# Optimization experiments

Hardware: AMD Instinct MI355X
Metric: run time of the kernel (lower is better)

The kernel has to match this reference:

```python
import jax, jax.numpy as jnp
import numpy as np
import math

B, S, D, H, DFF = 4, 2048, 1024, 16, 4096
DK = D // H
EPS = 1e-5

def setup_inputs() -> dict:
    key = jax.random.key(0)
    ks = jax.random.split(key, 16)
    s_d = 1.0 / math.sqrt(D)
    s_ff = 1.0 / math.sqrt(DFF)
    return {
        "x": jax.random.normal(ks[0], (B, S, D), jnp.float32),
        "wq": jax.random.uniform(ks[1], (D, D), jnp.float32, -s_d, s_d),
        "bq": jnp.zeros((D,), jnp.float32),
        "wk": jax.random.uniform(ks[2], (D, D), jnp.float32, -s_d, s_d),
        "bk": jnp.zeros((D,), jnp.float32),
        "wv": jax.random.uniform(ks[3], (D, D), jnp.float32, -s_d, s_d),
        "bv": jnp.zeros((D,), jnp.float32),
        "wo": jax.random.uniform(ks[4], (D, D), jnp.float32, -s_d, s_d),
        "bo": jnp.zeros((D,), jnp.float32),
        "w1": jax.random.uniform(ks[5], (DFF, D), jnp.float32, -s_d, s_d),
        "b1": jnp.zeros((DFF,), jnp.float32),
        "w2": jax.random.uniform(ks[6], (D, DFF), jnp.float32, -s_ff, s_ff),
        "b2": jnp.zeros((D,), jnp.float32),
        "ln1_g": jnp.ones((D,), jnp.float32),
        "ln1_b": jnp.zeros((D,), jnp.float32),
        "ln2_g": jnp.ones((D,), jnp.float32),
        "ln2_b": jnp.zeros((D,), jnp.float32),
    }

def _layernorm(x, g, b):
    mu = jnp.mean(x, axis=-1, keepdims=True)
    var = jnp.mean(jnp.square(x - mu), axis=-1, keepdims=True)
    return (x - mu) * jax.lax.rsqrt(var + EPS) * g + b

def reference(x, wq, bq, wk, bk, wv, bv, wo, bo, w1, b1, w2, b2, ln1_g, ln1_b, ln2_g, ln2_b):
    # Multi-head self-attention (dropout in eval mode -> identity).
    Q = (x @ wq.T + bq).reshape(B, S, H, DK).transpose(0, 2, 1, 3)  # (B,H,S,DK)
    K = (x @ wk.T + bk).reshape(B, S, H, DK).transpose(0, 2, 1, 3)
    V = (x @ wv.T + bv).reshape(B, S, H, DK).transpose(0, 2, 1, 3)
    scores = jnp.einsum('bhqd,bhkd->bhqk', Q, K) / math.sqrt(DK)  # (B,H,S,S)
    attn = jax.nn.softmax(scores, axis=-1)
    ctx = jnp.einsum('bhqk,bhkd->bhqd', attn, V)
    ctx = ctx.transpose(0, 2, 1, 3).reshape(B, S, D)
    attn_out = ctx @ wo.T + bo
    # SkipConnection: x + norm(sublayer)  (post-applied LayerNorm on sublayer output)
    x = x + _layernorm(attn_out, ln1_g, ln1_b)
    # FFN
    ff = jax.nn.relu(x @ w1.T + b1) @ w2.T + b2
    return x + _layernorm(ff, ln2_g, ln2_b)
```

## Files before the change

kernel.cpp:

```cpp
#include <hip/hip_runtime.h>
#include <hip/hip_bf16.h>
#include <stdint.h>


#define DI __device__ __forceinline__

typedef __attribute__((ext_vector_type(4))) float f32x4;
typedef __attribute__((ext_vector_type(16))) float f32x16;
typedef __attribute__((ext_vector_type(8))) short bf16x8;
typedef __attribute__((ext_vector_type(4))) short s16x4;

#define B_ 4
#define S_ 2048
#define D_ 1024
#define H_ 16
#define DK_ 64
#define DFF_ 4096
#define M_ 8192

DI float bf2f(short s) {
  union { unsigned u; float f; } v;
  v.u = ((unsigned)(unsigned short)s) << 16;
  return v.f;
}
DI short f2bf(float f) {
  union { float f; unsigned u; } v;
  v.f = f;
  unsigned r = v.u + 0x7FFFu + ((v.u >> 16) & 1u);
  return (short)(r >> 16);
}
DI unsigned pkbf(float lo, float hi) {
  unsigned r;
  asm("v_cvt_pk_bf16_f32 %0, %1, %2" : "=v"(r) : "v"(lo), "v"(hi));
  return r;
}
DI void plswap(unsigned& a, unsigned& b) {
  asm volatile("v_permlane32_swap_b32 %0, %1" : "+v"(a), "+v"(b));
}
DI float ex2(float x) {
  float r;
  asm("v_exp_f32 %0, %1" : "=v"(r) : "v"(x));
  return r;
}

__global__ __launch_bounds__(256) void cvt_kernel(const float* __restrict__ in,
                                                  short* __restrict__ out, int n) {
  long i = ((long)blockIdx.x * blockDim.x + threadIdx.x) * 8;
  if (i >= n) return;
  f32x4 a = *(const f32x4*)(in + i);
  f32x4 b = *(const f32x4*)(in + i + 4);
  bf16x8 r;
  r[0] = f2bf(a[0]); r[1] = f2bf(a[1]); r[2] = f2bf(a[2]); r[3] = f2bf(a[3]);
  r[4] = f2bf(b[0]); r[5] = f2bf(b[1]); r[6] = f2bf(b[2]); r[7] = f2bf(b[3]);
  *(bf16x8*)(out + i) = r;
}

DI void gl_lds16(const void* g, void* l) {
  __builtin_amdgcn_global_load_lds(
      (const __attribute__((address_space(1))) unsigned int*)g,
      (__attribute__((address_space(3))) unsigned int*)l, 16, 0, 0);
}

template <int BN, int MODE>
__global__ __launch_bounds__(512, 2)
void gemm_qs(const short* __restrict__ A, const short* __restrict__ Bm,
             const float* __restrict__ bias0, const float* __restrict__ bias1,
             const float* __restrict__ bias2, short* __restrict__ C,
             int M, int N, int K,
             short* __restrict__ Qo, short* __restrict__ Ko, short* __restrict__ Vo) {
  constexpr int NF = BN / 64;
  constexpr int WN = BN / 4;
  constexpr int ASLOT = 256 * 32;
  constexpr int BSLOT = BN * 32;

  __shared__ short As[4 * ASLOT];
  __shared__ short Bs[4 * BSLOT];

  const int t = threadIdx.x, w = t >> 6, l = t & 63;
  const int wm = w >> 2, wn = w & 3;
  const int lr = l & 15, lk = l >> 4;

  const int gx = gridDim.x;
  const int nwg = gx * gridDim.y;
  const int orig = blockIdx.y * gx + blockIdx.x;
  const int lin = (orig & 7) * (nwg >> 3) + (orig >> 3);
  const int row0 = (lin / gx) * 256;
  const int col0 = (lin % gx) * BN;

  const int NT = K >> 5;

  const int r0 = t >> 2, s0 = (((t & 3) ^ ((r0 >> 1) & 3)) << 3);
  const int r1 = r0 + 128, s1 = (((t & 3) ^ ((r1 >> 1) & 3)) << 3);
  const short* Asrc0 = A + (long)(row0 + r0) * K + s0;
  const short* Asrc1 = A + (long)(row0 + r1) * K + s1;
  const short* Bsrc0 = Bm + (long)(col0 + r0) * K + s0;
  const short* Bsrc1 = Bm + (long)(col0 + r1) * K + s1;
  const int d0 = t * 8, d1 = (t + 512) * 8;

  auto stageA = [&](int kt) {
    const int ko = kt << 5;
    short* Ab = As + (kt & 3) * ASLOT;
    gl_lds16(Asrc0 + ko, Ab + d0);
    gl_lds16(Asrc1 + ko, Ab + d1);
  };
  auto stageB = [&](int kt) {
    const int ko = kt << 5;
    short* Bb = Bs + (kt & 3) * BSLOT;
    gl_lds16(Bsrc0 + ko, Bb + d0);
    if constexpr (BN == 256) gl_lds16(Bsrc1 + ko, Bb + d1);
  };

  f32x4 acc[8][NF] = {};

  stageA(0); stageB(0);
  stageA(1); stageB(1);
  stageA(2); stageB(2);

  for (int kt = 0; kt < NT; ++kt) {
    if (kt + 2 < NT) {
      if constexpr (BN == 256) asm volatile("s_waitcnt vmcnt(8)" ::: "memory");
      else                     asm volatile("s_waitcnt vmcnt(6)" ::: "memory");
    } else if (kt + 1 < NT) {
      if constexpr (BN == 256) asm volatile("s_waitcnt vmcnt(4)" ::: "memory");
      else                     asm volatile("s_waitcnt vmcnt(3)" ::: "memory");
    } else {
      asm volatile("s_waitcnt vmcnt(0)" ::: "memory");
    }
    __builtin_amdgcn_s_barrier();

    const short* aw = As + (kt & 3) * ASLOT + wm * (128 * 32);
    const short* bw = Bs + (kt & 3) * BSLOT + wn * (WN * 32);

    bf16x8 afr[4], bfr[NF];
#pragma unroll
    for (int m = 0; m < 4; ++m) {
      const int rr = m * 16 + lr;
      afr[m] = *(const bf16x8*)(aw + rr * 32 + ((lk ^ ((rr >> 1) & 3)) << 3));
    }
#pragma unroll
    for (int n = 0; n < NF; ++n) {
      const int rr = n * 16 + lr;
      bfr[n] = *(const bf16x8*)(bw + rr * 32 + ((lk ^ ((rr >> 1) & 3)) << 3));
    }
    if (kt + 3 < NT) stageA(kt + 3);
    __builtin_amdgcn_s_barrier();
    asm volatile("s_waitcnt lgkmcnt(0)" ::: "memory");
    __builtin_amdgcn_sched_barrier(0);
    __builtin_amdgcn_s_setprio(1);
#pragma unroll
    for (int m = 0; m < 4; ++m)
#pragma unroll
      for (int n = 0; n < NF; ++n)
        acc[m][n] =
            __builtin_amdgcn_mfma_f32_16x16x32_bf16(afr[m], bfr[n], acc[m][n], 0, 0, 0);
    __builtin_amdgcn_s_setprio(0);

    bf16x8 af2[4];
#pragma unroll
    for (int m = 0; m < 4; ++m) {
      const int rr = 64 + m * 16 + lr;
      af2[m] = *(const bf16x8*)(aw + rr * 32 + ((lk ^ ((rr >> 1) & 3)) << 3));
    }
    if (kt + 3 < NT) stageB(kt + 3);
    __builtin_amdgcn_s_barrier();
    asm volatile("s_waitcnt lgkmcnt(0)" ::: "memory");
    __builtin_amdgcn_sched_barrier(0);
    __builtin_amdgcn_s_setprio(1);
#pragma unroll
    for (int m = 0; m < 4; ++m)
#pragma unroll
      for (int n = 0; n < NF; ++n)
        acc[4 + m][n] =
            __builtin_amdgcn_mfma_f32_16x16x32_bf16(af2[m], bfr[n], acc[4 + m][n], 0, 0, 0);
    __builtin_amdgcn_s_setprio(0);
  }

  if (MODE == 2) {
    const int which = col0 >> 10;
#pragma unroll
    for (int m = 0; m < 8; ++m) {
#pragma unroll
      for (int n = 0; n < NF; ++n) {
        const int r0e = row0 + wm * 128 + m * 16 + lk * 4;
        const int c = col0 + wn * WN + n * 16 + lr;
        const int cc = c & 1023;
        const int h = cc >> 6, dk = cc & 63;
        const int bb = r0e >> 11, s = r0e & 2047;
        if (which == 2) {
          const float bias = bias2[cc];
          s16x4 v4;
#pragma unroll
          for (int j = 0; j < 4; ++j) v4[j] = f2bf(acc[m][n][j] + bias);
          *(s16x4*)(Vo + ((long)((bb * H_ + h) * DK_ + dk)) * S_ + s) = v4;
        } else {
          const float bias = (which == 0 ? bias0[cc] : bias1[cc]);
          const float sc = (which == 0 ? 0.1803368801f : 1.0f);
          short* dst = (which == 0 ? Qo : Ko);
#pragma unroll
          for (int j = 0; j < 4; ++j)
            dst[(((long)(bb * H_ + h) * S_) + s + j) * DK_ + dk] =
                f2bf((acc[m][n][j] + bias) * sc);
        }
      }
    }
  } else {
#pragma unroll
    for (int m = 0; m < 8; ++m) {
#pragma unroll
      for (int n = 0; n < NF; ++n) {
#pragma unroll
        for (int j = 0; j < 4; ++j) {
          const int r = row0 + wm * 128 + m * 16 + lk * 4 + j;
          const int c = col0 + wn * WN + n * 16 + lr;
          float v = acc[m][n][j] + bias0[c];
          if (MODE == 1) v = fmaxf(v, 0.0f);
          C[(long)r * N + c] = f2bf(v);
        }
      }
    }
  }
}

__global__ __launch_bounds__(256, 4)
void attn_kernel(const short* __restrict__ Q, const short* __restrict__ K,
                 const short* __restrict__ Vt, short* __restrict__ ctx) {
  __shared__ short Ks[2 * 64 * 64];
  __shared__ short Vs[2 * 64 * 64];
  const int t = threadIdx.x, w = t >> 6, l = t & 63;
  const int q31 = l & 31, hi = l >> 5;
  const int bh = blockIdx.y;
  const int q0 = blockIdx.x * 128 + w * 32;
  const long base = (long)bh * S_ * DK_;

  bf16x8 qf[4];
  {
    const short* qp = Q + base + (long)(q0 + q31) * DK_ + hi * 8;
#pragma unroll
    for (int ks = 0; ks < 4; ++ks) qf[ks] = *(const bf16x8*)(qp + ks * 16);
  }

  f32x16 oa[2] = {};
  float mrun = -1e30f, lrun = 0.0f;

  const int srow = l >> 3;
  const int scol = ((l & 7) ^ srow) * 8;
  const int kr0 = w * 16 + srow, kr1 = w * 16 + 8 + srow;
  const int lw0 = w * 1024, lw1 = w * 1024 + 512;

  gl_lds16(K + base + (long)kr0 * DK_ + scol, &Ks[lw0]);
  gl_lds16(K + base + (long)kr1 * DK_ + scol, &Ks[lw1]);
  gl_lds16(Vt + base + (long)kr0 * S_ + scol, &Vs[lw0]);
  gl_lds16(Vt + base + (long)kr1 * S_ + scol, &Vs[lw1]);

  for (int tt = 0; tt < 32; ++tt) {
    asm volatile("s_waitcnt vmcnt(0)" ::: "memory");
    __builtin_amdgcn_s_barrier();
    if (tt + 1 < 32) {
      const int kb = ((tt + 1) & 1) * 4096;
      const int kvn = (tt + 1) * 64;
      gl_lds16(K + base + (long)(kvn + kr0) * DK_ + scol, &Ks[kb + lw0]);
      gl_lds16(K + base + (long)(kvn + kr1) * DK_ + scol, &Ks[kb + lw1]);
      gl_lds16(Vt + base + (long)kr0 * S_ + kvn + scol, &Vs[kb + lw0]);
      gl_lds16(Vt + base + (long)kr1 * S_ + kvn + scol, &Vs[kb + lw1]);
    }
    const int cb = (tt & 1) * 4096;

    f32x16 sacc[2] = {};
#pragma unroll
    for (int m = 0; m < 2; ++m) {
      const int row = m * 32 + q31;
      const int sw = row & 7;
#pragma unroll
      for (int ks = 0; ks < 4; ++ks) {
        bf16x8 kf = *(const bf16x8*)&Ks[cb + row * 64 + (((2 * ks + hi) ^ sw) << 3)];
        sacc[m] = __builtin_amdgcn_mfma_f32_32x32x16_bf16(kf, qf[ks], sacc[m], 0, 0, 0);
      }
    }

    float mx[8];
#pragma unroll
    for (int r = 0; r < 8; ++r)
      mx[r] = fmaxf(fmaxf(sacc[0][r], sacc[0][r + 8]),
                    fmaxf(sacc[1][r], sacc[1][r + 8]));
    mx[0] = fmaxf(mx[0], mx[4]); mx[1] = fmaxf(mx[1], mx[5]);
    mx[2] = fmaxf(mx[2], mx[6]); mx[3] = fmaxf(mx[3], mx[7]);
    float tm = fmaxf(fmaxf(mx[0], mx[1]), fmaxf(mx[2], mx[3]));
    tm = fmaxf(tm, __shfl_xor(tm, 32, 64));

    if (!__all(tm <= mrun + 8.0f)) {
      const float mnew = fmaxf(mrun, tm);
      const float fac = ex2(mrun - mnew);
      lrun *= fac;
#pragma unroll
      for (int m = 0; m < 2; ++m)
#pragma unroll
        for (int r = 0; r < 16; ++r) oa[m][r] *= fac;
      mrun = mnew;
    }

#pragma unroll
    for (int m = 0; m < 2; ++m)
#pragma unroll
      for (int r = 0; r < 16; ++r) sacc[m][r] = ex2(sacc[m][r] - mrun);

    float sm[8];
#pragma unroll
    for (int r = 0; r < 8; ++r)
      sm[r] = (sacc[0][r] + sacc[0][r + 8]) + (sacc[1][r] + sacc[1][r + 8]);
    sm[0] += sm[4]; sm[1] += sm[5]; sm[2] += sm[6]; sm[3] += sm[7];
    float ps = (sm[0] + sm[1]) + (sm[2] + sm[3]);
    ps += __shfl_xor(ps, 32, 64);
    lrun += ps;

    bf16x8 pf[4];
#pragma unroll
    for (int m = 0; m < 2; ++m)
#pragma unroll
      for (int sb = 0; sb < 2; ++sb) {
        unsigned p0 = pkbf(sacc[m][8 * sb + 0], sacc[m][8 * sb + 1]);
        unsigned p1 = pkbf(sacc[m][8 * sb + 2], sacc[m][8 * sb + 3]);
        unsigned p2 = pkbf(sacc[m][8 * sb + 4], sacc[m][8 * sb + 5]);
        unsigned p3 = pkbf(sacc[m][8 * sb + 6], sacc[m][8 * sb + 7]);
        plswap(p0, p2);
        plswap(p1, p3);
        union { unsigned u[4]; bf16x8 v; } fb;
        fb.u[0] = p0; fb.u[1] = p1; fb.u[2] = p2; fb.u[3] = p3;
        pf[2 * m + sb] = fb.v;
      }

#pragma unroll
    for (int mt = 0; mt < 2; ++mt) {
      const int row = mt * 32 + q31;
      const int sw = row & 7;
#pragma unroll
      for (int s = 0; s < 4; ++s) {
        bf16x8 vf = *(const bf16x8*)&Vs[cb + row * 64 + (((2 * s + hi) ^ sw) << 3)];
        oa[mt] = __builtin_amdgcn_mfma_f32_32x32x16_bf16(vf, pf[s], oa[mt], 0, 0, 0);
      }
    }
  }

  const int bb2 = bh >> 4, h = bh & 15;
  const float rl = 1.0f / lrun;
  short* crow = ctx + ((long)(bb2 * S_ + q0 + q31)) * D_ + h * 64 + 4 * hi;
#pragma unroll
  for (int mt = 0; mt < 2; ++mt)
#pragma unroll
    for (int g = 0; g < 4; ++g) {
      s16x4 v4;
#pragma unroll
      for (int i = 0; i < 4; ++i) v4[i] = f2bf(oa[mt][4 * g + i] * rl);
      *(s16x4*)(crow + mt * 32 + g * 8) = v4;
    }
}

template <int RES_BF16, int OUT_BF16>
__global__ __launch_bounds__(256)
void add_ln(const void* __restrict__ resv, const short* __restrict__ a,
            const float* __restrict__ gam, const float* __restrict__ bet,
            void* __restrict__ outv) {
  const int row = blockIdx.x, t = threadIdx.x;
  const int w = t >> 6, l = t & 63;
  const long roff = (long)row * D_;
  const int c = t * 4;
  s16x4 av = *(const s16x4*)(a + roff + c);
  float v0 = bf2f(av[0]), v1 = bf2f(av[1]), v2 = bf2f(av[2]), v3 = bf2f(av[3]);
  float s = v0 + v1 + v2 + v3;
#pragma unroll
  for (int mask = 1; mask < 64; mask <<= 1) s += __shfl_xor(s, mask, 64);
  __shared__ float r1[4], r2[4];
  if (l == 0) r1[w] = s;
  __syncthreads();
  float mu = (r1[0] + r1[1] + r1[2] + r1[3]) * (1.0f / D_);
  float d0 = v0 - mu, d1 = v1 - mu, d2 = v2 - mu, d3 = v3 - mu;
  float sq = d0 * d0 + d1 * d1 + d2 * d2 + d3 * d3;
#pragma unroll
  for (int mask = 1; mask < 64; mask <<= 1) sq += __shfl_xor(sq, mask, 64);
  if (l == 0) r2[w] = sq;
  __syncthreads();
  float var = (r2[0] + r2[1] + r2[2] + r2[3]) * (1.0f / D_);
  float rs = rsqrtf(var + 1e-5f);
  float res0, res1, res2, res3;
  if (RES_BF16) {
    s16x4 rv = *(const s16x4*)((const short*)resv + roff + c);
    res0 = bf2f(rv[0]); res1 = bf2f(rv[1]); res2 = bf2f(rv[2]); res3 = bf2f(rv[3]);
  } else {
    f32x4 rv = *(const f32x4*)((const float*)resv + roff + c);
    res0 = rv[0]; res1 = rv[1]; res2 = rv[2]; res3 = rv[3];
  }
  float o0 = res0 + d0 * rs * gam[c + 0] + bet[c + 0];
  float o1 = res1 + d1 * rs * gam[c + 1] + bet[c + 1];
  float o2 = res2 + d2 * rs * gam[c + 2] + bet[c + 2];
  float o3 = res3 + d3 * rs * gam[c + 3] + bet[c + 3];
  if (OUT_BF16) {
    s16x4 ov;
    ov[0] = f2bf(o0); ov[1] = f2bf(o1); ov[2] = f2bf(o2); ov[3] = f2bf(o3);
    *(s16x4*)((short*)outv + roff + c) = ov;
  } else {
    f32x4 ov;
    ov[0] = o0; ov[1] = o1; ov[2] = o2; ov[3] = o3;
    *(f32x4*)((float*)outv + roff + c) = ov;
  }
}

extern "C" void kernel_launch(void* const* d_in, const int* in_sizes, int n_in,
                              void* d_out, int out_size, void* d_ws, size_t ws_size,
                              hipStream_t stream) {
  (void)in_sizes; (void)n_in; (void)out_size; (void)ws_size;
  const float* x   = (const float*)d_in[0];
  const float* wq  = (const float*)d_in[1];
  const float* bq  = (const float*)d_in[2];
  const float* wk  = (const float*)d_in[3];
  const float* bk  = (const float*)d_in[4];
  const float* wv  = (const float*)d_in[5];
  const float* bv  = (const float*)d_in[6];
  const float* wo  = (const float*)d_in[7];
  const float* bo  = (const float*)d_in[8];
  const float* w1  = (const float*)d_in[9];
  const float* b1  = (const float*)d_in[10];
  const float* w2  = (const float*)d_in[11];
  const float* b2  = (const float*)d_in[12];
  const float* g1  = (const float*)d_in[13];
  const float* be1 = (const float*)d_in[14];
  const float* g2  = (const float*)d_in[15];
  const float* be2 = (const float*)d_in[16];

  char* ws = (char*)d_ws;
  const long MB = 1 << 20;
  short* xb    = (short*)(ws + 0 * MB);
  short* wqkvb = (short*)(ws + 16 * MB);
  short* wob   = (short*)(ws + 22 * MB);
  short* w1b   = (short*)(ws + 24 * MB);
  short* w2b   = (short*)(ws + 32 * MB);
  short* Qb    = (short*)(ws + 40 * MB);
  short* Kb    = (short*)(ws + 56 * MB);
  short* Vtb   = (short*)(ws + 72 * MB);
  short* ctxb  = (short*)(ws + 88 * MB);
  short* aout  = (short*)(ws + 40 * MB);
  short* x1b   = (short*)(ws + 56 * MB);
  short* hid   = (short*)(ws + 88 * MB);
  short* ffb   = (short*)(ws + 72 * MB);

  auto cvt = [&](const float* in, short* out, long n) {
    cvt_kernel<<<dim3((unsigned)((n / 8 + 255) / 256)), dim3(256), 0, stream>>>(in, out, (int)n);
  };
  cvt(x, xb, (long)M_ * D_);
  cvt(wq, wqkvb + 0L * D_ * D_, (long)D_ * D_);
  cvt(wk, wqkvb + 1L * D_ * D_, (long)D_ * D_);
  cvt(wv, wqkvb + 2L * D_ * D_, (long)D_ * D_);
  cvt(wo, wob, (long)D_ * D_);
  cvt(w1, w1b, (long)DFF_ * D_);
  cvt(w2, w2b, (long)D_ * DFF_);

  gemm_qs<256, 2><<<dim3(3072 / 256, M_ / 256), 512, 0, stream>>>(
      xb, wqkvb, bq, bk, bv, nullptr, M_, 3072, D_, Qb, Kb, Vtb);

  attn_kernel<<<dim3(S_ / 128, B_ * H_), 256, 0, stream>>>(Qb, Kb, Vtb, ctxb);

  gemm_qs<128, 0><<<dim3(D_ / 128, M_ / 256), 512, 0, stream>>>(
      ctxb, wob, bo, nullptr, nullptr, aout, M_, D_, D_, nullptr, nullptr, nullptr);

  add_ln<0, 1><<<dim3(M_), 256, 0, stream>>>(x, aout, g1, be1, x1b);

  gemm_qs<256, 1><<<dim3(DFF_ / 256, M_ / 256), 512, 0, stream>>>(
      x1b, w1b, b1, nullptr, nullptr, hid, M_, DFF_, D_, nullptr, nullptr, nullptr);
  gemm_qs<128, 0><<<dim3(D_ / 128, M_ / 256), 512, 0, stream>>>(
      hid, w2b, b2, nullptr, nullptr, ffb, M_, D_, DFF_, nullptr, nullptr, nullptr);

  add_ln<1, 0><<<dim3(M_), 256, 0, stream>>>(x1b, ffb, g2, be2, d_out);
}
```

Before: 419.5 us.

## Retile GEMM warp grid, enlarge attention blocks with XCD-aware mapping, use max3

For the BN=128 GEMMs the 8 waves are rearranged into a 4x2 grid, so each wave covers 64x64 instead of 128x32, which changes the balance of A and B fragment reads from LDS. The attention kernel moves to 512-thread blocks covering 256 queries, so each K/V tile staged in LDS is shared by twice as many waves. Its block index is remapped so that blocks of the same batch-head land on the same XCD, improving L2 reuse of K and V. The running-max reduction now uses v_max3_f32. The larger blocks raise per-block register and LDS pressure and may reduce the number of resident blocks.

Result: no change. 413.0 us (-1.5%).

```diff
diff --git a/kernel.cpp b/kernel.cpp
--- a/kernel.cpp
+++ b/kernel.cpp
@@ -40,6 +40,11 @@
 DI float ex2(float x) {
   float r;
   asm("v_exp_f32 %0, %1" : "=v"(r) : "v"(x));
+  return r;
+}
+DI float max3(float a, float b, float c) {
+  float r;
+  asm("v_max3_f32 %0, %1, %2, %3" : "=v"(r) : "v"(a), "v"(b), "v"(c));
   return r;
 }
 
@@ -61,6 +66,11 @@
       (__attribute__((address_space(3))) unsigned int*)l, 16, 0, 0);
 }
 
+#define VMCNT(N) asm volatile("s_waitcnt vmcnt(" #N ")" ::: "memory")
+#define LGKM0                                          \
+  asm volatile("s_waitcnt lgkmcnt(0)" ::: "memory");   \
+  __builtin_amdgcn_sched_barrier(0)
+
 template <int BN, int MODE>
 __global__ __launch_bounds__(512, 2)
 void gemm_qs(const short* __restrict__ A, const short* __restrict__ Bm,
@@ -68,8 +78,13 @@
              const float* __restrict__ bias2, short* __restrict__ C,
              int M, int N, int K,
              short* __restrict__ Qo, short* __restrict__ Ko, short* __restrict__ Vo) {
-  constexpr int NF = BN / 64;
-  constexpr int WN = BN / 4;
+  constexpr int WR = (BN == 256 ? 2 : 4);
+  constexpr int WC = 8 / WR;
+  constexpr int WM = 256 / WR;
+  constexpr int WN = BN / WC;
+  constexpr int MF = WM / 16;
+  constexpr int NFr = WN / 16;
+  constexpr int MH = MF / 2;
   constexpr int ASLOT = 256 * 32;
   constexpr int BSLOT = BN * 32;
 
@@ -77,7 +92,8 @@
   __shared__ short Bs[4 * BSLOT];
 
   const int t = threadIdx.x, w = t >> 6, l = t & 63;
-  const int wm = w >> 2, wn = w & 3;
+  const int wm = (WR == 2 ? (w >> 2) : (w >> 1));
+  const int wn = (WR == 2 ? (w & 3) : (w & 1));
   const int lr = l & 15, lk = l >> 4;
 
   const int gx = gridDim.x;
@@ -110,7 +126,7 @@
     if constexpr (BN == 256) gl_lds16(Bsrc1 + ko, Bb + d1);
   };
 
-  f32x4 acc[8][NF] = {};
+  f32x4 acc[MF][NFr] = {};
 
   stageA(0); stageB(0);
   stageA(1); stageB(1);
@@ -118,70 +134,66 @@
 
   for (int kt = 0; kt < NT; ++kt) {
     if (kt + 2 < NT) {
-      if constexpr (BN == 256) asm volatile("s_waitcnt vmcnt(8)" ::: "memory");
-      else                     asm volatile("s_waitcnt vmcnt(6)" ::: "memory");
+      if constexpr (BN == 256) VMCNT(8); else VMCNT(6);
     } else if (kt + 1 < NT) {
-      if constexpr (BN == 256) asm volatile("s_waitcnt vmcnt(4)" ::: "memory");
-      else                     asm volatile("s_waitcnt vmcnt(3)" ::: "memory");
+      if constexpr (BN == 256) VMCNT(4); else VMCNT(3);
     } else {
-      asm volatile("s_waitcnt vmcnt(0)" ::: "memory");
+      VMCNT(0);
     }
     __builtin_amdgcn_s_barrier();
 
-    const short* aw = As + (kt & 3) * ASLOT + wm * (128 * 32);
+    const short* aw = As + (kt & 3) * ASLOT + wm * (WM * 32);
     const short* bw = Bs + (kt & 3) * BSLOT + wn * (WN * 32);
 
-    bf16x8 afr[4], bfr[NF];
-#pragma unroll
-    for (int m = 0; m < 4; ++m) {
+    bf16x8 afr[MH], bfr[NFr];
+#pragma unroll
+    for (int m = 0; m < MH; ++m) {
       const int rr = m * 16 + lr;
       afr[m] = *(const bf16x8*)(aw + rr * 32 + ((lk ^ ((rr >> 1) & 3)) << 3));
     }
 #pragma unroll
-    for (int n = 0; n < NF; ++n) {
+    for (int n = 0; n < NFr; ++n) {
       const int rr = n * 16 + lr;
       bfr[n] = *(const bf16x8*)(bw + rr * 32 + ((lk ^ ((rr >> 1) & 3)) << 3));
     }
     if (kt + 3 < NT) stageA(kt + 3);
     __builtin_amdgcn_s_barrier();
-    asm volatile("s_waitcnt lgkmcnt(0)" ::: "memory");
-    __builtin_amdgcn_sched_barrier(0);
+    LGKM0;
     __builtin_amdgcn_s_setprio(1);
 #pragma unroll
-    for (int m = 0; m < 4; ++m)
-#pragma unroll
-      for (int n = 0; n < NF; ++n)
+    for (int m = 0; m < MH; ++m)
+#pragma unroll
+      for (int n = 0; n < NFr; ++n)
         acc[m][n] =
             __builtin_amdgcn_mfma_f32_16x16x32_bf16(afr[m], bfr[n], acc[m][n], 0, 0, 0);
     __builtin_amdgcn_s_setprio(0);
 
-    bf16x8 af2[4];
-#pragma unroll
-    for (int m = 0; m < 4; ++m) {
-      const int rr = 64 + m * 16 + lr;
+    bf16x8 af2[MH];
+#pragma unroll
+    for (int m = 0; m < MH; ++m) {
+      const int rr = (MH + m) * 16 + lr;
       af2[m] = *(const bf16x8*)(aw + rr * 32 + ((lk ^ ((rr >> 1) & 3)) << 3));
     }
     if (kt + 3 < NT) stageB(kt + 3);
     __builtin_amdgcn_s_barrier();
-    asm volatile("s_waitcnt lgkmcnt(0)" ::: "memory");
-    __builtin_amdgcn_sched_barrier(0);
+    LGKM0;
     __builtin_amdgcn_s_setprio(1);
 #pragma unroll
-    for (int m = 0; m < 4; ++m)
-#pragma unroll
-      for (int n = 0; n < NF; ++n)
-        acc[4 + m][n] =
-            __builtin_amdgcn_mfma_f32_16x16x32_bf16(af2[m], bfr[n], acc[4 + m][n], 0, 0, 0);
+    for (int m = 0; m < MH; ++m)
+#pragma unroll
+      for (int n = 0; n < NFr; ++n)
+        acc[MH + m][n] =
+            __builtin_amdgcn_mfma_f32_16x16x32_bf16(af2[m], bfr[n], acc[MH + m][n], 0, 0, 0);
     __builtin_amdgcn_s_setprio(0);
   }
 
   if (MODE == 2) {
     const int which = col0 >> 10;
 #pragma unroll
-    for (int m = 0; m < 8; ++m) {
-#pragma unroll
-      for (int n = 0; n < NF; ++n) {
-        const int r0e = row0 + wm * 128 + m * 16 + lk * 4;
+    for (int m = 0; m < MF; ++m) {
+#pragma unroll
+      for (int n = 0; n < NFr; ++n) {
+        const int r0e = row0 + wm * WM + m * 16 + lk * 4;
         const int c = col0 + wn * WN + n * 16 + lr;
         const int cc = c & 1023;
         const int h = cc >> 6, dk = cc & 63;
@@ -205,12 +217,12 @@
     }
   } else {
 #pragma unroll
-    for (int m = 0; m < 8; ++m) {
-#pragma unroll
-      for (int n = 0; n < NF; ++n) {
+    for (int m = 0; m < MF; ++m) {
+#pragma unroll
+      for (int n = 0; n < NFr; ++n) {
 #pragma unroll
         for (int j = 0; j < 4; ++j) {
-          const int r = row0 + wm * 128 + m * 16 + lk * 4 + j;
+          const int r = row0 + wm * WM + m * 16 + lk * 4 + j;
           const int c = col0 + wn * WN + n * 16 + lr;
           float v = acc[m][n][j] + bias0[c];
           if (MODE == 1) v = fmaxf(v, 0.0f);
@@ -221,15 +233,18 @@
   }
 }
 
-__global__ __launch_bounds__(256, 4)
+__global__ __launch_bounds__(512, 4)
 void attn_kernel(const short* __restrict__ Q, const short* __restrict__ K,
                  const short* __restrict__ Vt, short* __restrict__ ctx) {
-  __shared__ short Ks[2 * 64 * 64];
-  __shared__ short Vs[2 * 64 * 64];
+  __shared__ short Ks[2 * 4096];
+  __shared__ short Vs[2 * 4096];
   const int t = threadIdx.x, w = t >> 6, l = t & 63;
   const int q31 = l & 31, hi = l >> 5;
-  const int bh = blockIdx.y;
-  const int q0 = blockIdx.x * 128 + w * 32;
+
+  const int orig = blockIdx.y * gridDim.x + blockIdx.x;
+  const int xcd = orig & 7, k7 = orig >> 3;
+  const int bh = xcd * 8 + (k7 >> 3);
+  const int q0 = (k7 & 7) * 256 + w * 32;
   const long base = (long)bh * S_ * DK_;
 
   bf16x8 qf[4];
@@ -242,27 +257,24 @@
   f32x16 oa[2] = {};
   float mrun = -1e30f, lrun = 0.0f;
 
-  const int srow = l >> 3;
-  const int scol = ((l & 7) ^ srow) * 8;
-  const int kr0 = w * 16 + srow, kr1 = w * 16 + 8 + srow;
-  const int lw0 = w * 1024, lw1 = w * 1024 + 512;
-
-  gl_lds16(K + base + (long)kr0 * DK_ + scol, &Ks[lw0]);
-  gl_lds16(K + base + (long)kr1 * DK_ + scol, &Ks[lw1]);
-  gl_lds16(Vt + base + (long)kr0 * S_ + scol, &Vs[lw0]);
-  gl_lds16(Vt + base + (long)kr1 * S_ + scol, &Vs[lw1]);
+  const int trow = t >> 3;
+  const int tcol = (((t & 7) ^ (trow & 7)) << 3);
+  const short* Ksrc = K + base + (long)trow * DK_ + tcol;
+  const short* Vsrc = Vt + base + (long)trow * S_ + tcol;
+
+  auto stg = [&](int tile, int slot) {
+    const int kb = slot * 4096;
+    const int kvn = tile * 64;
+    gl_lds16(Ksrc + (long)kvn * DK_, &Ks[kb + t * 8]);
+    gl_lds16(Vsrc + kvn, &Vs[kb + t * 8]);
+  };
+
+  stg(0, 0);
 
   for (int tt = 0; tt < 32; ++tt) {
-    asm volatile("s_waitcnt vmcnt(0)" ::: "memory");
+    VMCNT(0);
     __builtin_amdgcn_s_barrier();
-    if (tt + 1 < 32) {
-      const int kb = ((tt + 1) & 1) * 4096;
-      const int kvn = (tt + 1) * 64;
-      gl_lds16(K + base + (long)(kvn + kr0) * DK_ + scol, &Ks[kb + lw0]);
-      gl_lds16(K + base + (long)(kvn + kr1) * DK_ + scol, &Ks[kb + lw1]);
-      gl_lds16(Vt + base + (long)kr0 * S_ + kvn + scol, &Vs[kb + lw0]);
-      gl_lds16(Vt + base + (long)kr1 * S_ + kvn + scol, &Vs[kb + lw1]);
-    }
+    if (tt + 1 < 32) stg(tt + 1, (tt + 1) & 1);
     const int cb = (tt & 1) * 4096;
 
     f32x16 sacc[2] = {};
@@ -280,11 +292,10 @@
     float mx[8];
 #pragma unroll
     for (int r = 0; r < 8; ++r)
-      mx[r] = fmaxf(fmaxf(sacc[0][r], sacc[0][r + 8]),
-                    fmaxf(sacc[1][r], sacc[1][r + 8]));
-    mx[0] = fmaxf(mx[0], mx[4]); mx[1] = fmaxf(mx[1], mx[5]);
-    mx[2] = fmaxf(mx[2], mx[6]); mx[3] = fmaxf(mx[3], mx[7]);
-    float tm = fmaxf(fmaxf(mx[0], mx[1]), fmaxf(mx[2], mx[3]));
+      mx[r] = fmaxf(max3(sacc[0][r], sacc[0][r + 8], sacc[1][r]), sacc[1][r + 8]);
+    float ma = max3(mx[0], mx[1], mx[2]);
+    float mb = max3(mx[3], mx[4], mx[5]);
+    float tm = fmaxf(max3(mx[6], mx[7], ma), mb);
     tm = fmaxf(tm, __shfl_xor(tm, 32, 64));
 
     if (!__all(tm <= mrun + 8.0f)) {
@@ -455,7 +466,7 @@
   gemm_qs<256, 2><<<dim3(3072 / 256, M_ / 256), 512, 0, stream>>>(
       xb, wqkvb, bq, bk, bv, nullptr, M_, 3072, D_, Qb, Kb, Vtb);
 
-  attn_kernel<<<dim3(S_ / 128, B_ * H_), 256, 0, stream>>>(Qb, Kb, Vtb, ctxb);
+  attn_kernel<<<dim3(S_ / 256, B_ * H_), 512, 0, stream>>>(Qb, Kb, Vtb, ctxb);
 
   gemm_qs<128, 0><<<dim3(D_ / 128, M_ / 256), 512, 0, stream>>>(
       ctxb, wob, bo, nullptr, nullptr, aout, M_, D_, D_, nullptr, nullptr, nullptr);
```
